# Performance work log

Hardware: AMD Instinct MI355X
Metric: run time of the kernel (lower is better)

The kernel has to match this reference:

```python
import jax, jax.numpy as jnp
import numpy as np

B_, T_, DIM = 32, 65536, 64
L_ = T_ // DIM                       # 1024 tokens after unfold
EXPAND, HEADDIM, DSTATE, DCONV = 4, 64, 16, 4
DIN = EXPAND * DIM                   # 256
NHEADS = DIN // HEADDIM              # 4
CONVDIM = DIN + 2 * DSTATE           # 288 (x, B, C share the conv)
DINPROJ = 2 * DIN + 2 * DSTATE + NHEADS  # 548
EPS = 1e-5


def setup_inputs() -> dict:
    key = jax.random.key(0)
    ks = jax.random.split(key, 8)
    x = jax.random.normal(ks[0], (B_, T_), jnp.float32)
    in_proj_w = jax.random.normal(ks[1], (DINPROJ, DIM), jnp.float32) * (DIM ** -0.5)
    conv_w = jax.random.normal(ks[2], (CONVDIM, DCONV), jnp.float32) * (DCONV ** -0.5)
    conv_b = jax.random.normal(ks[3], (CONVDIM,), jnp.float32) * 0.01
    # dt_bias so that softplus(dt_bias) ~ dt in [1e-3, 1e-1] (standard Mamba init)
    dt_bias = jnp.log(jnp.expm1(jax.random.uniform(ks[4], (NHEADS,), minval=0.001, maxval=0.1)))
    A_log = jnp.log(jax.random.uniform(ks[5], (NHEADS,), minval=1.0, maxval=16.0))
    D = jnp.ones((NHEADS,), jnp.float32)
    norm_gate_w = jnp.ones((DIN,), jnp.float32)
    out_proj_w = jax.random.normal(ks[6], (DIM, DIN), jnp.float32) * (DIN ** -0.5)
    block_norm_w = jnp.ones((DIM,), jnp.float32)
    return dict(x=x, in_proj_w=in_proj_w, conv_w=conv_w, conv_b=conv_b,
                dt_bias=dt_bias, A_log=A_log, D=D, norm_gate_w=norm_gate_w,
                out_proj_w=out_proj_w, block_norm_w=block_norm_w)


def _rmsnorm(x, w, eps=EPS):
    return x * jax.lax.rsqrt(jnp.mean(x * x, axis=-1, keepdims=True) + eps) * w


def _mamba2(u, in_proj_w, conv_w, conv_b, dt_bias, A_log, D, norm_gate_w, out_proj_w):
    # u: (b, l, d_model)
    b, l, _ = u.shape
    zxbcdt = jnp.einsum('bld,ed->ble', u, in_proj_w)            # (b,l,548)
    z, xBC, dt = jnp.split(zxbcdt, [DIN, DIN + CONVDIM], axis=-1)
    dt = jax.nn.softplus(dt + dt_bias)                           # (b,l,h)
    # causal depthwise conv1d (kernel DCONV) + SiLU
    xp = jnp.pad(xBC, ((0, 0), (DCONV - 1, 0), (0, 0)))
    xc = conv_b + sum(xp[:, k:k + l, :] * conv_w[:, k] for k in range(DCONV))
    xBC = jax.nn.silu(xc)
    xs, Bm, Cm = jnp.split(xBC, [DIN, DIN + DSTATE], axis=-1)    # (b,l,256),(b,l,16),(b,l,16)
    xh = xs.reshape(b, l, NHEADS, HEADDIM)                       # (b,l,h,p)
    A = -jnp.exp(A_log)                                          # (h,)

    def step(h, inp):
        x_t, dt_t, B_t, C_t = inp                                # (b,h,p),(b,h),(b,n),(b,n)
        dA = jnp.exp(dt_t * A)                                   # (b,h)
        h = h * dA[..., None, None] + dt_t[..., None, None] * x_t[..., None] * B_t[:, None, None, :]
        y = jnp.einsum('bhpn,bn->bhp', h, C_t)
        return h, y

    h0 = jnp.zeros((b, NHEADS, HEADDIM, DSTATE), u.dtype)
    _, ys = jax.lax.scan(step, h0, (xh.transpose(1, 0, 2, 3), dt.transpose(1, 0, 2),
                                    Bm.transpose(1, 0, 2), Cm.transpose(1, 0, 2)))
    y = ys.transpose(1, 0, 2, 3) + D[:, None] * xh               # (b,l,h,p) skip term
    y = y.reshape(b, l, DIN)
    y = _rmsnorm(y * jax.nn.silu(z), norm_gate_w)                # RMSNormGated
    return jnp.einsum('ble,de->bld', y, out_proj_w)              # (b,l,d_model)


def reference(x, in_proj_w, conv_w, conv_b, dt_bias, A_log, D, norm_gate_w,
              out_proj_w, block_norm_w):
    B, T = x.shape
    batch = x.reshape(B, L_, DIM)                                # unfold(1, dim, dim)
    # Block(fused_add_norm=False, n_layer=1): residual=batch; hidden=mixer(norm(batch))
    hidden = _mamba2(_rmsnorm(batch, block_norm_w), in_proj_w, conv_w, conv_b,
                     dt_bias, A_log, D, norm_gate_w, out_proj_w)
    residual = hidden + batch                                    # forward_f + for_residual
    out = residual.reshape(B, T) + x                             # flatten + input residual
    return out
```

## Files before the change

### kernel.cpp

```cpp
#include <hip/hip_runtime.h>
#include <math.h>

#define BB 32
#define LL 1024
#define DIMM 64
#define DINN 256
#define NHEADS 4
#define DSTATE 16
#define DINPROJ 548
#define EPSF 1e-5f
#define NCH 16
#define CS 64

typedef __attribute__((ext_vector_type(8))) short bf16x8;
typedef __attribute__((ext_vector_type(4))) float f32x4;

__device__ inline ushort f2bf(float f) {
    union { float f; unsigned u; } v; v.f = f;
    unsigned r = (v.u + 0x7FFFu + ((v.u >> 16) & 1u)) >> 16;
    return (ushort)r;
}
__device__ inline float bf2f(ushort u) {
    union { float f; unsigned u; } v; v.u = ((unsigned)u) << 16; return v.f;
}
__device__ inline float fexp(float v) { return __expf(v); }
__device__ inline float fsilu(float v) {
    return v * __builtin_amdgcn_rcpf(1.f + __expf(-v));
}

__global__ __launch_bounds__(256) void kwcvt(
        const float* __restrict__ Win, const float* __restrict__ Wout,
        ushort* __restrict__ Wb, ushort* __restrict__ Wob) {
    int i = blockIdx.x * 256 + threadIdx.x;
    if (i < DINPROJ * 64) Wb[i] = f2bf(Win[i]);
    else if (i < DINPROJ * 64 + 64 * DINN) {
        int j = i - DINPROJ * 64;
        Wob[j] = f2bf(Wout[j]);
    }
}

__global__ __launch_bounds__(256) void k1_mfma(
        const float* __restrict__ x, const ushort* __restrict__ Wb,
        const float* __restrict__ bnw, const float* __restrict__ Wfp,
        const float* __restrict__ dt_bias,
        ushort* __restrict__ zbuf, ushort* __restrict__ xbcbuf,
        float* __restrict__ dtbuf) {
    __shared__ __align__(16) union {
        struct { float u[32][68]; float wdt[4][68]; } a;
        ushort ob[32][552];
    } s;
    __shared__ float rstd[32];
    const int t = threadIdx.x;
    const int m0 = blockIdx.x * 32;
    const int b = m0 >> 10;
    const int lbase = m0 & 1023;

    const float* xrow = x + (size_t)m0 * 64;
    #pragma unroll
    for (int i = 0; i < 2; ++i) {
        int idx = t + i * 256;
        float4 v = ((const float4*)xrow)[idx];
        *(float4*)&s.a.u[idx >> 4][(idx & 15) * 4] = v;
    }
    s.a.wdt[t >> 6][t & 63] = Wfp[(size_t)(544 + (t >> 6)) * 64 + (t & 63)] * bnw[t & 63];
    __syncthreads();
    {
        int row = t >> 3, part = t & 7;
        float ss = 0.f;
        #pragma unroll
        for (int j = 0; j < 8; ++j) { float v = s.a.u[row][part * 8 + j]; ss = fmaf(v, v, ss); }
        ss += __shfl_xor(ss, 1); ss += __shfl_xor(ss, 2); ss += __shfl_xor(ss, 4);
        if (part == 0) rstd[row] = rsqrtf(ss * (1.f / 64.f) + EPSF);
    }
    __syncthreads();

    const int w = t >> 6, l = t & 63;
    const int a = l & 15, kb = (l >> 4) * 8;

    float4 bw[2][2];
    bw[0][0] = *(const float4*)&bnw[kb];
    bw[0][1] = *(const float4*)&bnw[kb + 4];
    bw[1][0] = *(const float4*)&bnw[32 + kb];
    bw[1][1] = *(const float4*)&bnw[32 + kb + 4];

    bf16x8 af[2][2];
    #pragma unroll
    for (int mt = 0; mt < 2; ++mt) {
        float rs = rstd[mt * 16 + a];
        #pragma unroll
        for (int kk = 0; kk < 2; ++kk) {
            float4 v0 = *(const float4*)&s.a.u[mt * 16 + a][kk * 32 + kb];
            float4 v1 = *(const float4*)&s.a.u[mt * 16 + a][kk * 32 + kb + 4];
            ushort* p = (ushort*)&af[mt][kk];
            p[0] = f2bf(v0.x * rs * bw[kk][0].x);
            p[1] = f2bf(v0.y * rs * bw[kk][0].y);
            p[2] = f2bf(v0.z * rs * bw[kk][0].z);
            p[3] = f2bf(v0.w * rs * bw[kk][0].w);
            p[4] = f2bf(v1.x * rs * bw[kk][1].x);
            p[5] = f2bf(v1.y * rs * bw[kk][1].y);
            p[6] = f2bf(v1.z * rs * bw[kk][1].z);
            p[7] = f2bf(v1.w * rs * bw[kk][1].w);
        }
    }

    if (t < 128) {
        int row = t >> 2, h = t & 3;
        const float* ur = s.a.u[row];
        const float* wr = s.a.wdt[h];
        float sd = 0.f;
        #pragma unroll
        for (int k4 = 0; k4 < 16; ++k4) {
            float4 uv = *(const float4*)&ur[k4 * 4];
            float4 wv = *(const float4*)&wr[k4 * 4];
            sd = fmaf(uv.x, wv.x, sd); sd = fmaf(uv.y, wv.y, sd);
            sd = fmaf(uv.z, wv.z, sd); sd = fmaf(uv.w, wv.w, sd);
        }
        sd = sd * rstd[row] + dt_bias[h];
        sd = fmaxf(sd, 0.f) + log1pf(expf(-fabsf(sd)));
        dtbuf[((size_t)(b * 4 + h)) * LL + lbase + row] = sd;
    }
    __syncthreads();

    for (int nt = w; nt < 34; nt += 4) {
        const ushort* wbp = Wb + (size_t)(nt * 16 + a) * 64 + kb;
        bf16x8 b0 = *(const bf16x8*)wbp;
        bf16x8 b1 = *(const bf16x8*)(wbp + 32);
        #pragma unroll
        for (int mt = 0; mt < 2; ++mt) {
            f32x4 acc = {0.f, 0.f, 0.f, 0.f};
            acc = __builtin_amdgcn_mfma_f32_16x16x32_bf16(af[mt][0], b0, acc, 0, 0, 0);
            acc = __builtin_amdgcn_mfma_f32_16x16x32_bf16(af[mt][1], b1, acc, 0, 0, 0);
            int row0 = mt * 16 + (l >> 4) * 4;
            int col = nt * 16 + a;
            if (nt < 16) {
                #pragma unroll
                for (int r = 0; r < 4; ++r) s.ob[row0 + r][col] = f2bf(fsilu(acc[r]));
            } else {
                #pragma unroll
                for (int r = 0; r < 4; ++r) s.ob[row0 + r][col] = f2bf(acc[r]);
            }
        }
    }
    __syncthreads();

    for (int i = t; i < 1024; i += 256) {
        int row = i >> 5, c8 = (i & 31) * 8;
        *(uint4*)&zbuf[(size_t)(m0 + row) * DINN + c8] = *(const uint4*)&s.ob[row][c8];
    }
    for (int i = t; i < 1152; i += 256) {
        int row = i / 36, c8 = (i % 36) * 8;
        *(uint4*)&xbcbuf[(size_t)(m0 + row) * 288 + c8] = *(const uint4*)&s.ob[row][256 + c8];
    }
}

__global__ __launch_bounds__(256) void k3a_ssd(
        const ushort* __restrict__ xbcbuf, const float* __restrict__ dtbuf,
        const float* __restrict__ conv_w, const float* __restrict__ conv_b,
        const float* __restrict__ A_log, const float* __restrict__ Dp,
        ushort* __restrict__ y, float* __restrict__ h0buf,
        float* __restrict__ cdecbuf, ushort* __restrict__ Cpost) {
    const int bid = blockIdx.x;
    const int c = bid & 15, h = (bid >> 4) & 3, b = bid >> 6;
    const int t = threadIdx.x;

    __shared__ __align__(16) union {
        struct { ushort rawx[67][64]; ushort rawbc[67][32]; } st;
        struct { ushort Mb[64][72]; ushort BwT[16][72]; } ssd;
    } uu;
    __shared__ ushort XbT[64][72];
    __shared__ ushort Bb[64][40];
    __shared__ ushort Cb[64][40];
    __shared__ float dtt[64], laa[64], ww[64];

    const float A  = -expf(A_log[h]);
    const float Dh = Dp[h];
    const int l0 = c * CS;
    const ushort* xb = xbcbuf + (size_t)b * LL * 288;

    for (int i = t; i < 67 * 32; i += 256) {
        int r = i >> 5, cu = i & 31;
        int l = l0 - 3 + r;
        ((uint*)&uu.st.rawx[r][0])[cu] =
            (l >= 0) ? ((const uint*)(xb + (size_t)l * 288 + h * 64))[cu] : 0u;
    }
    for (int i = t; i < 67 * 16; i += 256) {
        int r = i >> 4, cu = i & 15;
        int l = l0 - 3 + r;
        ((uint*)&uu.st.rawbc[r][0])[cu] =
            (l >= 0) ? ((const uint*)(xb + (size_t)l * 288 + 256))[cu] : 0u;
    }
    for (int i = t; i < 512; i += 256) {
        int r = i >> 3, cc = i & 7;
        ((uint*)&Bb[r][16])[cc] = 0;
        ((uint*)&Cb[r][16])[cc] = 0;
    }
    if (t < 64) {
        float dv = dtbuf[((size_t)(b * 4 + h)) * LL + l0 + t];
        float run = dv * A;
        #pragma unroll
        for (int off = 1; off < 64; off <<= 1) {
            float o = __shfl_up(run, off, 64);
            if (t >= off) run += o;
        }
        dtt[t] = dv;
        laa[t] = run;
        cdecbuf[((size_t)(b * 4 + h)) * LL + l0 + t] = fexp(run);
        float laEnd = __shfl(run, 63, 64);
        ww[t] = dv * fexp(laEnd - run);
    }
    __syncthreads();

    {
        const int jx = t & 63;
        const int w0 = (t >> 6) * 16;
        const int cx = h * 64 + jx;
        const float4 cwx = *(const float4*)&conv_w[cx * 4];
        const float  cbx = conv_b[cx];
        float r0[19];
        #pragma unroll
        for (int k = 0; k < 19; ++k) r0[k] = bf2f(uu.st.rawx[w0 + k][jx]);
        ushort vv[16];
        #pragma unroll
        for (int k = 0; k < 16; ++k) {
            float v = cbx + r0[k] * cwx.x + r0[k + 1] * cwx.y
                          + r0[k + 2] * cwx.z + r0[k + 3] * cwx.w;
            vv[k] = f2bf(fsilu(v));
        }
        *(bf16x8*)&XbT[jx][w0]     = *(bf16x8*)&vv[0];
        *(bf16x8*)&XbT[jx][w0 + 8] = *(bf16x8*)&vv[8];

        const int jbc = t & 31, cbc = 256 + jbc;
        const float4 cwb = *(const float4*)&conv_w[cbc * 4];
        const float  cbb = conv_b[cbc];
        #pragma unroll
        for (int i = 0; i < 8; ++i) {
            int ss = (t >> 5) + i * 8;
            float v = cbb + bf2f(uu.st.rawbc[ss][jbc]) * cwb.x
                          + bf2f(uu.st.rawbc[ss + 1][jbc]) * cwb.y
                          + bf2f(uu.st.rawbc[ss + 2][jbc]) * cwb.z
                          + bf2f(uu.st.rawbc[ss + 3][jbc]) * cwb.w;
            v = fsilu(v);
            if (jbc < 16) Bb[ss][jbc] = f2bf(v);
            else {
                ushort bv = f2bf(v);
                Cb[ss][jbc - 16] = bv;
                Cpost[((size_t)b * LL + l0 + ss) * DSTATE + (jbc - 16)] = bv;
            }
        }
    }
    __syncthreads();

    const int w = t >> 6, l = t & 63;
    const int fr = l & 15, fq = l >> 4;

    f32x4 gacc[4];
    {
        bf16x8 ca = *(const bf16x8*)&Cb[w * 16 + fr][fq * 8];
        #pragma unroll
        for (int jt = 0; jt < 4; ++jt) {
            bf16x8 bb = *(const bf16x8*)&Bb[jt * 16 + fr][fq * 8];
            f32x4 z = {0.f, 0.f, 0.f, 0.f};
            gacc[jt] = __builtin_amdgcn_mfma_f32_16x16x32_bf16(ca, bb, z, 0, 0, 0);
        }
    }
    #pragma unroll
    for (int jt = 0; jt < 4; ++jt) {
        int j = jt * 16 + fr;
        float laj = laa[j], dtj = dtt[j];
        #pragma unroll
        for (int r = 0; r < 4; ++r) {
            int i = w * 16 + fq * 4 + r;
            float m = (j <= i) ? gacc[jt][r] * fexp(laa[i] - laj) * dtj : 0.f;
            uu.ssd.Mb[i][j] = f2bf(m);
        }
    }
    #pragma unroll
    for (int i2 = 0; i2 < 4; ++i2) {
        int idx = t + i2 * 256;
        int n = idx & 15, jj = idx >> 4;
        uu.ssd.BwT[n][jj] = f2bf(ww[jj] * bf2f(Bb[jj][n]));
    }

    {
        bf16x8 ma0 = *(const bf16x8*)&uu.ssd.Mb[w * 16 + fr][fq * 8];
        bf16x8 ma1 = *(const bf16x8*)&uu.ssd.Mb[w * 16 + fr][32 + fq * 8];
        #pragma unroll
        for (int pt = 0; pt < 4; ++pt) {
            bf16x8 xb0 = *(const bf16x8*)&XbT[pt * 16 + fr][fq * 8];
            bf16x8 xb1 = *(const bf16x8*)&XbT[pt * 16 + fr][32 + fq * 8];
            f32x4 acc = {0.f, 0.f, 0.f, 0.f};
            acc = __builtin_amdgcn_mfma_f32_16x16x32_bf16(ma0, xb0, acc, 0, 0, 0);
            acc = __builtin_amdgcn_mfma_f32_16x16x32_bf16(ma1, xb1, acc, 0, 0, 0);
            #pragma unroll
            for (int r = 0; r < 4; ++r) {
                int i = w * 16 + fq * 4 + r;
                int p = pt * 16 + fr;
                float xv = bf2f(XbT[p][i]);
                uu.ssd.Mb[i][p] = f2bf(acc[r] + Dh * xv);
            }
        }
    }
    __syncthreads();

    if (c < 15) {
        bf16x8 xa0 = *(const bf16x8*)&XbT[w * 16 + fr][fq * 8];
        bf16x8 xa1 = *(const bf16x8*)&XbT[w * 16 + fr][32 + fq * 8];
        bf16x8 bw0 = *(const bf16x8*)&uu.ssd.BwT[fr][fq * 8];
        bf16x8 bw1 = *(const bf16x8*)&uu.ssd.BwT[fr][32 + fq * 8];
        f32x4 acc = {0.f, 0.f, 0.f, 0.f};
        acc = __builtin_amdgcn_mfma_f32_16x16x32_bf16(xa0, bw0, acc, 0, 0, 0);
        acc = __builtin_amdgcn_mfma_f32_16x16x32_bf16(xa1, bw1, acc, 0, 0, 0);
        float* Sdst = h0buf + (((size_t)(b * 4 + h)) * NCH + (c + 1)) * 1024;
        #pragma unroll
        for (int r = 0; r < 4; ++r) {
            int p = w * 16 + fq * 4 + r;
            Sdst[p * 16 + fr] = acc[r];
        }
    }

    {
        ushort* ybase = y + ((size_t)b * LL + l0) * DINN + h * 64;
        #pragma unroll
        for (int ii = 0; ii < 2; ++ii) {
            int idx = t + ii * 256;
            int row = idx >> 3, c8 = (idx & 7) * 8;
            *(uint4*)&ybase[(size_t)row * DINN + c8] = *(const uint4*)&uu.ssd.Mb[row][c8];
        }
    }
}

__global__ __launch_bounds__(256) void k3b_chunkscan(
        float* __restrict__ h0buf, const float* __restrict__ cdecbuf) {
    const int bh = blockIdx.x;
    const int t = threadIdx.x;
    float* base = h0buf + (size_t)bh * NCH * 1024;
    const float* cd = cdecbuf + (size_t)bh * LL;
    float4 run = {0.f, 0.f, 0.f, 0.f};
    *(float4*)&base[(size_t)t * 4] = run;
    #pragma unroll
    for (int c = 1; c < NCH; ++c) {
        float P = cd[c * CS - 1];
        float4 S = *(float4*)&base[(size_t)c * 1024 + t * 4];
        run.x = fmaf(run.x, P, S.x);
        run.y = fmaf(run.y, P, S.y);
        run.z = fmaf(run.z, P, S.z);
        run.w = fmaf(run.w, P, S.w);
        *(float4*)&base[(size_t)c * 1024 + t * 4] = run;
    }
}

__global__ __launch_bounds__(256) void k4_out(
        const ushort* __restrict__ ybf, const ushort* __restrict__ zbuf,
        const float* __restrict__ ngw, const ushort* __restrict__ Wob,
        const float* __restrict__ x, const float* __restrict__ h0buf,
        const float* __restrict__ cdecbuf, const ushort* __restrict__ Cpost,
        float* __restrict__ out) {
    __shared__ float Cs[64][16];
    __shared__ float cds[64][4];
    __shared__ ushort gb[64][264];
    const int t = threadIdx.x;
    const int m0 = blockIdx.x * 64;
    const int b  = m0 >> 10;
    const int l0 = m0 & 1023;
    const int ck = l0 >> 6;
    const ushort* yb = ybf + (size_t)m0 * DINN;
    const ushort* zb = zbuf + (size_t)m0 * DINN;

    {
        int r = t >> 2, n0 = (t & 3) * 4;
        ushort4 cu4 = *(const ushort4*)&Cpost[((size_t)b * LL + l0 + r) * DSTATE + n0];
        Cs[r][n0 + 0] = bf2f(cu4.x);
        Cs[r][n0 + 1] = bf2f(cu4.y);
        Cs[r][n0 + 2] = bf2f(cu4.z);
        Cs[r][n0 + 3] = bf2f(cu4.w);
        int hh2 = t & 3;
        cds[r][hh2] = cdecbuf[((size_t)(b * 4 + hh2)) * LL + l0 + r];
    }

    const int ch4 = (t & 63) * 4;
    const int hh  = ch4 >> 6;
    const int p0  = ch4 & 63;
    const float* hbase = h0buf + (((size_t)(b * 4 + hh)) * NCH + ck) * 1024 + p0 * 16;
    float4 H[4][4];
    #pragma unroll
    for (int k = 0; k < 4; ++k)
        #pragma unroll
        for (int n4 = 0; n4 < 4; ++n4)
            H[k][n4] = *(const float4*)&hbase[k * 16 + n4 * 4];
    __syncthreads();

    const float4 ng4 = *(const float4*)&ngw[ch4];

    #pragma unroll
    for (int i = 0; i < 16; ++i) {
        int row = i * 4 + (t >> 6);
        ushort4 yu = *(const ushort4*)&yb[(size_t)row * DINN + ch4];
        ushort4 zu = *(const ushort4*)&zb[(size_t)row * DINN + ch4];
        float4 yv = { bf2f(yu.x), bf2f(yu.y), bf2f(yu.z), bf2f(yu.w) };
        float4 zv = { bf2f(zu.x), bf2f(zu.y), bf2f(zu.z), bf2f(zu.w) };
        float4 C0 = *(const float4*)&Cs[row][0];
        float4 C1 = *(const float4*)&Cs[row][4];
        float4 C2 = *(const float4*)&Cs[row][8];
        float4 C3 = *(const float4*)&Cs[row][12];
        float cdv = cds[row][hh];
        float corr[4];
        #pragma unroll
        for (int k = 0; k < 4; ++k) {
            float s = H[k][0].x * C0.x + H[k][0].y * C0.y + H[k][0].z * C0.z + H[k][0].w * C0.w;
            s += H[k][1].x * C1.x + H[k][1].y * C1.y + H[k][1].z * C1.z + H[k][1].w * C1.w;
            s += H[k][2].x * C2.x + H[k][2].y * C2.y + H[k][2].z * C2.z + H[k][2].w * C2.w;
            s += H[k][3].x * C3.x + H[k][3].y * C3.y + H[k][3].z * C3.z + H[k][3].w * C3.w;
            corr[k] = s * cdv;
        }
        float4 gv;
        gv.x = (yv.x + corr[0]) * zv.x;
        gv.y = (yv.y + corr[1]) * zv.y;
        gv.z = (yv.z + corr[2]) * zv.z;
        gv.w = (yv.w + corr[3]) * zv.w;
        float s = gv.x * gv.x + gv.y * gv.y + gv.z * gv.z + gv.w * gv.w;
        s += __shfl_xor(s, 1);  s += __shfl_xor(s, 2);  s += __shfl_xor(s, 4);
        s += __shfl_xor(s, 8);  s += __shfl_xor(s, 16); s += __shfl_xor(s, 32);
        float rs = rsqrtf(s * (1.f / 256.f) + EPSF);
        ushort4 o;
        o.x = f2bf(gv.x * rs * ng4.x);
        o.y = f2bf(gv.y * rs * ng4.y);
        o.z = f2bf(gv.z * rs * ng4.z);
        o.w = f2bf(gv.w * rs * ng4.w);
        *(ushort4*)&gb[row][ch4] = o;
    }
    __syncthreads();

    const int w = t >> 6, l = t & 63;
    const int j = l & 15, kb = (l >> 4) * 8;
    bf16x8 bf[8];
    #pragma unroll
    for (int ks = 0; ks < 8; ++ks)
        bf[ks] = *(const bf16x8*)&Wob[(size_t)(16 * w + j) * DINN + ks * 32 + kb];
    #pragma unroll
    for (int mt = 0; mt < 4; ++mt) {
        f32x4 acc = {0.f, 0.f, 0.f, 0.f};
        #pragma unroll
        for (int ks = 0; ks < 8; ++ks) {
            bf16x8 af = *(const bf16x8*)&gb[mt * 16 + j][ks * 32 + kb];
            acc = __builtin_amdgcn_mfma_f32_16x16x32_bf16(af, bf[ks], acc, 0, 0, 0);
        }
        #pragma unroll
        for (int r = 0; r < 4; ++r) {
            size_t row = (size_t)m0 + mt * 16 + (l >> 4) * 4 + r;
            size_t oidx = row * 64 + 16 * w + j;
            out[oidx] = acc[r] + 2.f * x[oidx];
        }
    }
}

extern "C" void kernel_launch(void* const* d_in, const int* in_sizes, int n_in,
                              void* d_out, int out_size, void* d_ws, size_t ws_size,
                              hipStream_t stream) {
    const float* x          = (const float*)d_in[0];
    const float* in_proj_w  = (const float*)d_in[1];
    const float* conv_w     = (const float*)d_in[2];
    const float* conv_b     = (const float*)d_in[3];
    const float* dt_bias    = (const float*)d_in[4];
    const float* A_log      = (const float*)d_in[5];
    const float* D          = (const float*)d_in[6];
    const float* norm_gate  = (const float*)d_in[7];
    const float* out_proj_w = (const float*)d_in[8];
    const float* block_norm = (const float*)d_in[9];
    float* out = (float*)d_out;

    float* h0b   = (float*)d_ws;
    float* cdec  = h0b  + (size_t)BB * NHEADS * NCH * 1024;
    float* dtb   = cdec + (size_t)BB * NHEADS * LL;
    ushort* Cp   = (ushort*)(dtb + (size_t)BB * NHEADS * LL);
    ushort* ybf  = Cp   + (size_t)BB * LL * DSTATE;
    ushort* zbuf = ybf  + (size_t)BB * LL * DINN;
    ushort* xbc  = zbuf + (size_t)BB * LL * DINN;
    ushort* Wb   = xbc  + (size_t)BB * LL * 288;
    ushort* Wob  = Wb   + (size_t)DINPROJ * 64;

    kwcvt<<<201, 256, 0, stream>>>(in_proj_w, out_proj_w, Wb, Wob);
    k1_mfma<<<1024, 256, 0, stream>>>(x, Wb, block_norm, in_proj_w, dt_bias, zbuf, xbc, dtb);
    k3a_ssd<<<2048, 256, 0, stream>>>(xbc, dtb, conv_w, conv_b, A_log, D, ybf, h0b, cdec, Cp);
    k3b_chunkscan<<<128, 256, 0, stream>>>(h0b, cdec);
    k4_out<<<512, 256, 0, stream>>>(ybf, zbuf, norm_gate, Wob, x, h0b, cdec, Cp, out);
}
```

Baseline: 70.32 us.

## Recompute z gate projection in output kernel instead of storing zbuf

Moves the z-branch of the input projection (first 256 output columns, with SiLU) from k1 into k4. k4 now reloads x, recomputes the block RMSNorm and runs the z GEMM with MFMA into shared memory. This removes the bf16 z write and read through global memory (16 MB each way). In exchange, k4 does extra GEMM work and loads x twice, and its larger shared-memory footprint may reduce occupancy.

New measurement: 68.98 us. About the same (-1.9%).

```diff
diff --git a/kernel.cpp b/kernel.cpp
--- a/kernel.cpp
+++ b/kernel.cpp
@@ -43,11 +43,10 @@
         const float* __restrict__ x, const ushort* __restrict__ Wb,
         const float* __restrict__ bnw, const float* __restrict__ Wfp,
         const float* __restrict__ dt_bias,
-        ushort* __restrict__ zbuf, ushort* __restrict__ xbcbuf,
-        float* __restrict__ dtbuf) {
+        ushort* __restrict__ xbcbuf, float* __restrict__ dtbuf) {
     __shared__ __align__(16) union {
         struct { float u[32][68]; float wdt[4][68]; } a;
-        ushort ob[32][552];
+        ushort ob[32][296];
     } s;
     __shared__ float rstd[32];
     const int t = threadIdx.x;
@@ -121,7 +120,7 @@
     }
     __syncthreads();
 
-    for (int nt = w; nt < 34; nt += 4) {
+    for (int nt = 16 + w; nt < 34; nt += 4) {
         const ushort* wbp = Wb + (size_t)(nt * 16 + a) * 64 + kb;
         bf16x8 b0 = *(const bf16x8*)wbp;
         bf16x8 b1 = *(const bf16x8*)(wbp + 32);
@@ -131,25 +130,16 @@
             acc = __builtin_amdgcn_mfma_f32_16x16x32_bf16(af[mt][0], b0, acc, 0, 0, 0);
             acc = __builtin_amdgcn_mfma_f32_16x16x32_bf16(af[mt][1], b1, acc, 0, 0, 0);
             int row0 = mt * 16 + (l >> 4) * 4;
-            int col = nt * 16 + a;
-            if (nt < 16) {
-                #pragma unroll
-                for (int r = 0; r < 4; ++r) s.ob[row0 + r][col] = f2bf(fsilu(acc[r]));
-            } else {
-                #pragma unroll
-                for (int r = 0; r < 4; ++r) s.ob[row0 + r][col] = f2bf(acc[r]);
-            }
-        }
-    }
-    __syncthreads();
-
-    for (int i = t; i < 1024; i += 256) {
-        int row = i >> 5, c8 = (i & 31) * 8;
-        *(uint4*)&zbuf[(size_t)(m0 + row) * DINN + c8] = *(const uint4*)&s.ob[row][c8];
-    }
+            int col = nt * 16 + a - 256;
+            #pragma unroll
+            for (int r = 0; r < 4; ++r) s.ob[row0 + r][col] = f2bf(acc[r]);
+        }
+    }
+    __syncthreads();
+
     for (int i = t; i < 1152; i += 256) {
         int row = i / 36, c8 = (i % 36) * 8;
-        *(uint4*)&xbcbuf[(size_t)(m0 + row) * 288 + c8] = *(const uint4*)&s.ob[row][256 + c8];
+        *(uint4*)&xbcbuf[(size_t)(m0 + row) * 288 + c8] = *(const uint4*)&s.ob[row][c8];
     }
 }
 
@@ -350,22 +340,43 @@
 }
 
 __global__ __launch_bounds__(256) void k4_out(
-        const ushort* __restrict__ ybf, const ushort* __restrict__ zbuf,
-        const float* __restrict__ ngw, const ushort* __restrict__ Wob,
-        const float* __restrict__ x, const float* __restrict__ h0buf,
-        const float* __restrict__ cdecbuf, const ushort* __restrict__ Cpost,
-        float* __restrict__ out) {
+        const ushort* __restrict__ ybf, const float* __restrict__ ngw,
+        const ushort* __restrict__ Wob, const ushort* __restrict__ Wb,
+        const float* __restrict__ bnw, const float* __restrict__ x,
+        const float* __restrict__ h0buf, const float* __restrict__ cdecbuf,
+        const ushort* __restrict__ Cpost, float* __restrict__ out) {
+    __shared__ __align__(16) union {
+        float u[64][68];
+        ushort zg[64][264];
+    } s;
     __shared__ float Cs[64][16];
     __shared__ float cds[64][4];
-    __shared__ ushort gb[64][264];
+    __shared__ float rstd[64];
     const int t = threadIdx.x;
     const int m0 = blockIdx.x * 64;
     const int b  = m0 >> 10;
     const int l0 = m0 & 1023;
     const int ck = l0 >> 6;
     const ushort* yb = ybf + (size_t)m0 * DINN;
-    const ushort* zb = zbuf + (size_t)m0 * DINN;
-
+
+    const int ch4 = (t & 63) * 4;
+    const int hh  = ch4 >> 6;
+    const int p0  = ch4 & 63;
+    const float* hbase = h0buf + (((size_t)(b * 4 + hh)) * NCH + ck) * 1024 + p0 * 16;
+    float4 H[4][4];
+    #pragma unroll
+    for (int k = 0; k < 4; ++k)
+        #pragma unroll
+        for (int n4 = 0; n4 < 4; ++n4)
+            H[k][n4] = *(const float4*)&hbase[k * 16 + n4 * 4];
+
+    const float* xrow = x + (size_t)m0 * 64;
+    #pragma unroll
+    for (int i = 0; i < 4; ++i) {
+        int idx = t + i * 256;
+        float4 v = ((const float4*)xrow)[idx];
+        *(float4*)&s.u[idx >> 4][(idx & 15) * 4] = v;
+    }
     {
         int r = t >> 2, n0 = (t & 3) * 4;
         ushort4 cu4 = *(const ushort4*)&Cpost[((size_t)b * LL + l0 + r) * DSTATE + n0];
@@ -376,17 +387,63 @@
         int hh2 = t & 3;
         cds[r][hh2] = cdecbuf[((size_t)(b * 4 + hh2)) * LL + l0 + r];
     }
-
-    const int ch4 = (t & 63) * 4;
-    const int hh  = ch4 >> 6;
-    const int p0  = ch4 & 63;
-    const float* hbase = h0buf + (((size_t)(b * 4 + hh)) * NCH + ck) * 1024 + p0 * 16;
-    float4 H[4][4];
-    #pragma unroll
-    for (int k = 0; k < 4; ++k)
-        #pragma unroll
-        for (int n4 = 0; n4 < 4; ++n4)
-            H[k][n4] = *(const float4*)&hbase[k * 16 + n4 * 4];
+    __syncthreads();
+
+    {
+        int row = t >> 2, part = t & 3;
+        float ss = 0.f;
+        #pragma unroll
+        for (int j = 0; j < 16; ++j) { float v = s.u[row][part * 16 + j]; ss = fmaf(v, v, ss); }
+        ss += __shfl_xor(ss, 1); ss += __shfl_xor(ss, 2);
+        if (part == 0) rstd[row] = rsqrtf(ss * (1.f / 64.f) + EPSF);
+    }
+    __syncthreads();
+
+    const int w = t >> 6, l = t & 63;
+    const int a = l & 15, kb = (l >> 4) * 8;
+    float4 bw[2][2];
+    bw[0][0] = *(const float4*)&bnw[kb];
+    bw[0][1] = *(const float4*)&bnw[kb + 4];
+    bw[1][0] = *(const float4*)&bnw[32 + kb];
+    bw[1][1] = *(const float4*)&bnw[32 + kb + 4];
+    bf16x8 af[4][2];
+    #pragma unroll
+    for (int mt = 0; mt < 4; ++mt) {
+        float rs = rstd[mt * 16 + a];
+        #pragma unroll
+        for (int kk = 0; kk < 2; ++kk) {
+            float4 v0 = *(const float4*)&s.u[mt * 16 + a][kk * 32 + kb];
+            float4 v1 = *(const float4*)&s.u[mt * 16 + a][kk * 32 + kb + 4];
+            ushort* p = (ushort*)&af[mt][kk];
+            p[0] = f2bf(v0.x * rs * bw[kk][0].x);
+            p[1] = f2bf(v0.y * rs * bw[kk][0].y);
+            p[2] = f2bf(v0.z * rs * bw[kk][0].z);
+            p[3] = f2bf(v0.w * rs * bw[kk][0].w);
+            p[4] = f2bf(v1.x * rs * bw[kk][1].x);
+            p[5] = f2bf(v1.y * rs * bw[kk][1].y);
+            p[6] = f2bf(v1.z * rs * bw[kk][1].z);
+            p[7] = f2bf(v1.w * rs * bw[kk][1].w);
+        }
+    }
+    __syncthreads();
+
+    #pragma unroll
+    for (int ct4 = 0; ct4 < 4; ++ct4) {
+        int ct = w * 4 + ct4;
+        const ushort* wbp = Wb + (size_t)(ct * 16 + a) * 64 + kb;
+        bf16x8 b0 = *(const bf16x8*)wbp;
+        bf16x8 b1 = *(const bf16x8*)(wbp + 32);
+        #pragma unroll
+        for (int mt = 0; mt < 4; ++mt) {
+            f32x4 acc = {0.f, 0.f, 0.f, 0.f};
+            acc = __builtin_amdgcn_mfma_f32_16x16x32_bf16(af[mt][0], b0, acc, 0, 0, 0);
+            acc = __builtin_amdgcn_mfma_f32_16x16x32_bf16(af[mt][1], b1, acc, 0, 0, 0);
+            int row0 = mt * 16 + (l >> 4) * 4;
+            int col = ct * 16 + a;
+            #pragma unroll
+            for (int r = 0; r < 4; ++r) s.zg[row0 + r][col] = f2bf(fsilu(acc[r]));
+        }
+    }
     __syncthreads();
 
     const float4 ng4 = *(const float4*)&ngw[ch4];
@@ -395,7 +452,7 @@
     for (int i = 0; i < 16; ++i) {
         int row = i * 4 + (t >> 6);
         ushort4 yu = *(const ushort4*)&yb[(size_t)row * DINN + ch4];
-        ushort4 zu = *(const ushort4*)&zb[(size_t)row * DINN + ch4];
+        ushort4 zu = *(const ushort4*)&s.zg[row][ch4];
         float4 yv = { bf2f(yu.x), bf2f(yu.y), bf2f(yu.z), bf2f(yu.w) };
         float4 zv = { bf2f(zu.x), bf2f(zu.y), bf2f(zu.z), bf2f(zu.w) };
         float4 C0 = *(const float4*)&Cs[row][0];
@@ -406,32 +463,31 @@
         float corr[4];
         #pragma unroll
         for (int k = 0; k < 4; ++k) {
-            float s = H[k][0].x * C0.x + H[k][0].y * C0.y + H[k][0].z * C0.z + H[k][0].w * C0.w;
-            s += H[k][1].x * C1.x + H[k][1].y * C1.y + H[k][1].z * C1.z + H[k][1].w * C1.w;
-            s += H[k][2].x * C2.x + H[k][2].y * C2.y + H[k][2].z * C2.z + H[k][2].w * C2.w;
-            s += H[k][3].x * C3.x + H[k][3].y * C3.y + H[k][3].z * C3.z + H[k][3].w * C3.w;
-            corr[k] = s * cdv;
+            float sc = H[k][0].x * C0.x + H[k][0].y * C0.y + H[k][0].z * C0.z + H[k][0].w * C0.w;
+            sc += H[k][1].x * C1.x + H[k][1].y * C1.y + H[k][1].z * C1.z + H[k][1].w * C1.w;
+            sc += H[k][2].x * C2.x + H[k][2].y * C2.y + H[k][2].z * C2.z + H[k][2].w * C2.w;
+            sc += H[k][3].x * C3.x + H[k][3].y * C3.y + H[k][3].z * C3.z + H[k][3].w * C3.w;
+            corr[k] = sc * cdv;
         }
         float4 gv;
         gv.x = (yv.x + corr[0]) * zv.x;
         gv.y = (yv.y + corr[1]) * zv.y;
         gv.z = (yv.z + corr[2]) * zv.z;
         gv.w = (yv.w + corr[3]) * zv.w;
-        float s = gv.x * gv.x + gv.y * gv.y + gv.z * gv.z + gv.w * gv.w;
-        s += __shfl_xor(s, 1);  s += __shfl_xor(s, 2);  s += __shfl_xor(s, 4);
-        s += __shfl_xor(s, 8);  s += __shfl_xor(s, 16); s += __shfl_xor(s, 32);
-        float rs = rsqrtf(s * (1.f / 256.f) + EPSF);
+        float sq = gv.x * gv.x + gv.y * gv.y + gv.z * gv.z + gv.w * gv.w;
+        sq += __shfl_xor(sq, 1);  sq += __shfl_xor(sq, 2);  sq += __shfl_xor(sq, 4);
+        sq += __shfl_xor(sq, 8);  sq += __shfl_xor(sq, 16); sq += __shfl_xor(sq, 32);
+        float rs = rsqrtf(sq * (1.f / 256.f) + EPSF);
         ushort4 o;
         o.x = f2bf(gv.x * rs * ng4.x);
         o.y = f2bf(gv.y * rs * ng4.y);
         o.z = f2bf(gv.z * rs * ng4.z);
         o.w = f2bf(gv.w * rs * ng4.w);
-        *(ushort4*)&gb[row][ch4] = o;
-    }
-    __syncthreads();
-
-    const int w = t >> 6, l = t & 63;
-    const int j = l & 15, kb = (l >> 4) * 8;
+        *(ushort4*)&s.zg[row][ch4] = o;
+    }
+    __syncthreads();
+
+    const int j = l & 15;
     bf16x8 bf[8];
     #pragma unroll
     for (int ks = 0; ks < 8; ++ks)
@@ -441,8 +497,8 @@
         f32x4 acc = {0.f, 0.f, 0.f, 0.f};
         #pragma unroll
         for (int ks = 0; ks < 8; ++ks) {
-            bf16x8 af = *(const bf16x8*)&gb[mt * 16 + j][ks * 32 + kb];
-            acc = __builtin_amdgcn_mfma_f32_16x16x32_bf16(af, bf[ks], acc, 0, 0, 0);
+            bf16x8 ag = *(const bf16x8*)&s.zg[mt * 16 + j][ks * 32 + kb];
+            acc = __builtin_amdgcn_mfma_f32_16x16x32_bf16(ag, bf[ks], acc, 0, 0, 0);
         }
         #pragma unroll
         for (int r = 0; r < 4; ++r) {
@@ -473,14 +529,13 @@
     float* dtb   = cdec + (size_t)BB * NHEADS * LL;
     ushort* Cp   = (ushort*)(dtb + (size_t)BB * NHEADS * LL);
     ushort* ybf  = Cp   + (size_t)BB * LL * DSTATE;
-    ushort* zbuf = ybf  + (size_t)BB * LL * DINN;
-    ushort* xbc  = zbuf + (size_t)BB * LL * DINN;
+    ushort* xbc  = ybf  + (size_t)BB * LL * DINN;
     ushort* Wb   = xbc  + (size_t)BB * LL * 288;
     ushort* Wob  = Wb   + (size_t)DINPROJ * 64;
 
     kwcvt<<<201, 256, 0, stream>>>(in_proj_w, out_proj_w, Wb, Wob);
-    k1_mfma<<<1024, 256, 0, stream>>>(x, Wb, block_norm, in_proj_w, dt_bias, zbuf, xbc, dtb);
+    k1_mfma<<<1024, 256, 0, stream>>>(x, Wb, block_norm, in_proj_w, dt_bias, xbc, dtb);
     k3a_ssd<<<2048, 256, 0, stream>>>(xbc, dtb, conv_w, conv_b, A_log, D, ybf, h0b, cdec, Cp);
     k3b_chunkscan<<<128, 256, 0, stream>>>(h0b, cdec);
-    k4_out<<<512, 256, 0, stream>>>(ybf, zbuf, norm_gate, Wob, x, h0b, cdec, Cp, out);
-}
+    k4_out<<<512, 256, 0, stream>>>(ybf, norm_gate, Wob, Wb, block_norm, x, h0b, cdec, Cp, out);
+}
```
